# Optimization experiments

Hardware: AMD Instinct MI355X
Metric: run time of the kernel (lower is better)

## Reference

```python
import jax, jax.numpy as jnp
import numpy as np

# Tsit5 (Tsitouras 5(4)) Butcher tableau. 5th-order solution weights b == a7 row (FSAL).
A21 = 0.161
A31, A32 = -0.008480655492356989, 0.335480655492357
A41, A42, A43 = 2.8971530571054935, -6.359448489975075, 4.3622954328695815
A51, A52, A53, A54 = 5.325864828439257, -11.748883564062828, 7.4955393428898365, -0.09249506636175525
A61, A62, A63, A64, A65 = 5.86145544294642, -12.92096931784711, 8.159367898576159, -0.071584973281401, -0.028269050394068383
B1, B2, B3, B4, B5, B6 = 0.09646076681806523, 0.01, 0.4798896504144996, 1.379008574103742, -3.290069515436081, 2.324710524099774

B_TRAJ, D_STATE, D_FORCE, WIDTH = 1024, 256, 256, 512
T0, T1 = 0.0, 1.0
N_STEPS = 60  # fixed step h = DT0*SECOND = 60/3600 = 1/60 hour
H = (T1 - T0) / N_STEPS


def setup_inputs() -> dict:
    key = jax.random.key(0)
    ks = jax.random.split(key, 8)
    din = D_STATE + D_FORCE
    x0 = jax.random.normal(ks[0], (B_TRAJ, D_STATE), jnp.float32)
    u_forced = jax.random.normal(ks[1], (B_TRAJ, D_FORCE), jnp.float32) * 0.1
    W1 = jax.random.normal(ks[2], (WIDTH, din), jnp.float32) / np.sqrt(din)
    b1 = jnp.zeros((WIDTH,), jnp.float32)
    W2 = jax.random.normal(ks[3], (WIDTH, WIDTH), jnp.float32) / np.sqrt(WIDTH)
    b2 = jnp.zeros((WIDTH,), jnp.float32)
    W3 = jax.random.normal(ks[4], (D_STATE, WIDTH), jnp.float32) / np.sqrt(WIDTH)
    b3 = jnp.zeros((D_STATE,), jnp.float32)
    return dict(x0=x0, u_forced=u_forced, W1=W1, b1=b1, W2=W2, b2=b2, W3=W3, b3=b3)


def reference(x0, u_forced, W1, b1, W2, b2, W3, b3):
    # Augmented system: branch 0 = forced trajectory, branch 1 = unforced (zero force).
    # y: (2, B, D_STATE); u: (2, B, D_FORCE)
    y0 = jnp.stack([x0, x0])
    u = jnp.stack([u_forced, jnp.zeros_like(u_forced)])

    def mlp(z):  # z: (2, B, din) -> (2, B, D_STATE); eqx.nn.MLP default relu
        h = jax.nn.relu(jnp.einsum('kbi,oi->kbo', z, W1) + b1)
        h = jax.nn.relu(jnp.einsum('kbi,oi->kbo', h, W2) + b2)
        return jnp.einsum('kbi,oi->kbo', h, W3) + b3

    def f(y):  # ForcedVectorField: mlp(hstack((x, u))) on both branches at once
        return mlp(jnp.concatenate([y, u], axis=-1))

    def tsit5_step(y, _):
        k1 = f(y)
        k2 = f(y + H * (A21 * k1))
        k3 = f(y + H * (A31 * k1 + A32 * k2))
        k4 = f(y + H * (A41 * k1 + A42 * k2 + A43 * k3))
        k5 = f(y + H * (A51 * k1 + A52 * k2 + A53 * k3 + A54 * k4))
        k6 = f(y + H * (A61 * k1 + A62 * k2 + A63 * k3 + A64 * k4 + A65 * k5))
        y_new = y + H * (B1 * k1 + B2 * k2 + B3 * k3 + B4 * k4 + B5 * k5 + B6 * k6)
        return y_new, None

    y_final, _ = jax.lax.scan(jax.checkpoint(tsit5_step), y0, None, length=N_STEPS)
    # (forced_state, unforced_state) at t1, stacked: (2, B, D_STATE)
    return y_final
```

## Files before the change

kernel.cpp:

```cpp
#include <hip/hip_runtime.h>
#include <hip/hip_bf16.h>

typedef short  short8  __attribute__((ext_vector_type(8)));
typedef float  float4v __attribute__((ext_vector_type(4)));

#define NSTEPS 60
#define ROWS   16
#define GRID   128
#define C1S    518

constexpr double Hd = 1.0 / 60.0;
constexpr float HA1[1] = { (float)(Hd * 0.161) };
constexpr float HA2[2] = { (float)(Hd * -0.008480655492356989), (float)(Hd * 0.335480655492357) };
constexpr float HA3[3] = { (float)(Hd * 2.8971530571054935), (float)(Hd * -6.359448489975075),
                           (float)(Hd * 4.3622954328695815) };
constexpr float HA4[4] = { (float)(Hd * 5.325864828439257), (float)(Hd * -11.748883564062828),
                           (float)(Hd * 7.4955393428898365), (float)(Hd * -0.09249506636175525) };
constexpr float HA5[5] = { (float)(Hd * 5.86145544294642), (float)(Hd * -12.92096931784711),
                           (float)(Hd * 8.159367898576159), (float)(Hd * -0.071584973281401),
                           (float)(Hd * -0.028269050394068383) };
constexpr float HB6[6] = { (float)(Hd * 0.09646076681806523), (float)(Hd * 0.01),
                           (float)(Hd * 0.4798896504144996), (float)(Hd * 1.379008574103742),
                           (float)(Hd * -3.290069515436081), (float)(Hd * 2.324710524099774) };

__device__ __forceinline__ unsigned short f2bf(float f) {
    union { float f; unsigned u; } v; v.f = f;
    unsigned r = v.u + 0x7fffu + ((v.u >> 16) & 1u);
    return (unsigned short)(r >> 16);
}

__global__ void wconv(const float* __restrict__ W1, const float* __restrict__ W2,
                      const float* __restrict__ W3, unsigned short* __restrict__ ws) {
    int g = blockIdx.x * blockDim.x + threadIdx.x;
    int blk = g >> 6, l = g & 63;
    const float* src;
    if (blk < 256) {
        int b = blk; int nt = b >> 3, ks = b & 7;
        int n = nt * 16 + (l & 15), k = ks * 32 + (l >> 4) * 8;
        src = W1 + n * 512 + k;
    } else if (blk < 768) {
        int b = blk - 256; int nt = b >> 4, ks = b & 15;
        int n = nt * 16 + (l & 15), k = ks * 32 + (l >> 4) * 8;
        src = W2 + n * 512 + k;
    } else {
        int b = blk - 768; int nt = b >> 4, ks = b & 15;
        int n = nt * 16 + (l & 15), k = ks * 32 + (l >> 4) * 8;
        src = W3 + n * 512 + k;
    }
    short8 v;
#pragma unroll
    for (int j = 0; j < 8; ++j) v[j] = (short)f2bf(src[j]);
    *(((short8*)ws) + g) = v;
}

template<int KDIM, int NT>
__device__ __forceinline__ void mfma_block(const unsigned short* __restrict__ lds, int stride,
                                           const short8* __restrict__ wb, int ntg0, int lane,
                                           float4v* acc) {
    constexpr int KS = KDIM / 32;
    const int row  = lane & 15;
    const int koff = (lane >> 4) * 8;
    const int rm   = (row & 7) << 3;
    const short8* wp = wb + (size_t)ntg0 * KS * 64 + lane;
    short8 a_cur = *(const short8*)(lds + row * stride + (koff ^ rm));
    short8 b_cur[NT];
#pragma unroll
    for (int nt = 0; nt < NT; ++nt) b_cur[nt] = wp[(size_t)nt * KS * 64];
#pragma unroll
    for (int ks = 0; ks < KS; ++ks) {
        short8 a_nxt;
        short8 b_nxt[NT];
        if (ks + 1 < KS) {
            a_nxt = *(const short8*)(lds + row * stride + (((ks + 1) * 32 + koff) ^ rm));
#pragma unroll
            for (int nt = 0; nt < NT; ++nt) b_nxt[nt] = wp[((size_t)nt * KS + ks + 1) * 64];
        }
#pragma unroll
        for (int nt = 0; nt < NT; ++nt)
            acc[nt] = __builtin_amdgcn_mfma_f32_16x16x32_bf16(a_cur, b_cur[nt], acc[nt], 0, 0, 0);
        a_cur = a_nxt;
#pragma unroll
        for (int nt = 0; nt < NT; ++nt) b_cur[nt] = b_nxt[nt];
    }
}

__global__ void __launch_bounds__(512, 1) odeint(
        const float* __restrict__ x0, const float* __restrict__ uf,
        const float* __restrict__ W1, const float* __restrict__ b1,
        const float* __restrict__ b2, const float* __restrict__ b3,
        const unsigned short* __restrict__ ws, float* __restrict__ out) {
    __shared__ unsigned short xb[16 * 256];
    __shared__ unsigned short h1[16 * 512];
    __shared__ unsigned short h2[16 * 512];
    __shared__ float c1s[16 * C1S];
    __shared__ float bias2[512];
    __shared__ float bias3[256];

    const int tid  = threadIdx.x;
    const int wave = tid >> 6, lane = tid & 63;
    const int r0   = blockIdx.x * ROWS;

    float* utmp = (float*)h1;
    {
        const bool forced = (r0 < 1024);
        float4v* ud = (float4v*)utmp;
        for (int i = tid; i < ROWS * 64; i += 512) {
            int row = i >> 6, c4 = i & 63;
            float4v v = {0.f, 0.f, 0.f, 0.f};
            if (forced) v = *(const float4v*)(uf + (size_t)(r0 + row) * 256 + c4 * 4);
            ud[i] = v;
        }
    }
    bias2[tid] = b2[tid];
    if (tid < 256) bias3[tid] = b3[tid];
    __syncthreads();

    {
        int n = tid;
        float acc16[ROWS];
        float bb = b1[n];
#pragma unroll
        for (int r = 0; r < ROWS; ++r) acc16[r] = bb;
        const float* wrow = W1 + n * 512 + 256;
        for (int k = 0; k < 256; ++k) {
            float w = wrow[k];
#pragma unroll
            for (int r = 0; r < ROWS; ++r) acc16[r] += w * utmp[r * 256 + k];
        }
#pragma unroll
        for (int r = 0; r < ROWS; ++r) c1s[r * C1S + n] = acc16[r];
    }
    __syncthreads();

    float ybr[8];
    float kreg[6][8];
#pragma unroll
    for (int e = 0; e < 8; ++e) {
        int nt = e >> 2, r = e & 3;
        int row = (lane >> 4) * 4 + r;
        int n   = (wave * 2 + nt) * 16 + (lane & 15);
        ybr[e] = x0[(size_t)((r0 + row) & 1023) * 256 + n];
    }

    const short8* wy1 = (const short8*)ws;
    const short8* w2  = (const short8*)(ws + 131072);
    const short8* w3  = (const short8*)(ws + 393216);

#define DO_STAGE(S, COEF) do {                                                          \
    {                \
        _Pragma("unroll")                                                               \
        for (int e = 0; e < 8; ++e) {                                                   \
            int nt_ = e >> 2, r_ = e & 3;                                               \
            int row_ = (lane >> 4) * 4 + r_;                                            \
            int n_   = (wave * 2 + nt_) * 16 + (lane & 15);                             \
            float v_ = ybr[e];                                                          \
            _Pragma("unroll")                                                           \
            for (int j = 0; j < S; ++j) v_ += COEF[j] * kreg[j][e];                     \
            xb[row_ * 256 + (n_ ^ ((row_ & 7) << 3))] = f2bf(v_);                       \
        }                                                                               \
    }                                                                                   \
    __syncthreads();                                                   \
    {                                      \
        float4v a1[4];                                                                  \
        _Pragma("unroll") for (int q = 0; q < 4; ++q) a1[q] = (float4v){0.f,0.f,0.f,0.f}; \
        mfma_block<256, 4>(xb, 256, wy1, wave * 4, lane, a1);                           \
        _Pragma("unroll")                                                               \
        for (int nt = 0; nt < 4; ++nt) {                                                \
            int n_g = (wave * 4 + nt) * 16 + (lane & 15);                               \
            _Pragma("unroll")                                                           \
            for (int r = 0; r < 4; ++r) {                                               \
                int row = (lane >> 4) * 4 + r;                                          \
                float v = a1[nt][r] + c1s[row * C1S + n_g];                             \
                v = fmaxf(v, 0.f);                                                      \
                h1[row * 512 + (n_g ^ ((row & 7) << 3))] = f2bf(v);                     \
            }                                                                           \
        }                                                                               \
    }                                                                                   \
    __syncthreads();                                                   \
    {    \
        float4v a2[4];                                                                  \
        _Pragma("unroll") for (int q = 0; q < 4; ++q) a2[q] = (float4v){0.f,0.f,0.f,0.f}; \
        mfma_block<512, 4>(h1, 512, w2, wave * 4, lane, a2);                            \
        _Pragma("unroll")                                                               \
        for (int nt = 0; nt < 4; ++nt) {                                                \
            int n_g = (wave * 4 + nt) * 16 + (lane & 15);                               \
            _Pragma("unroll")                                                           \
            for (int r = 0; r < 4; ++r) {                                               \
                int row = (lane >> 4) * 4 + r;                                          \
                float v = a2[nt][r] + bias2[n_g];                                       \
                v = fmaxf(v, 0.f);                                                      \
                h2[row * 512 + (n_g ^ ((row & 7) << 3))] = f2bf(v);                     \
            }                                                                           \
        }                                                                               \
    }                                                                                   \
    __syncthreads();   \
    {        \
        float4v a3[2];                                                                  \
        _Pragma("unroll") for (int q = 0; q < 2; ++q) a3[q] = (float4v){0.f,0.f,0.f,0.f}; \
        mfma_block<512, 2>(h2, 512, w3, wave * 2, lane, a3);                            \
        _Pragma("unroll")                                                               \
        for (int nt = 0; nt < 2; ++nt) {                                                \
            int n_g = (wave * 2 + nt) * 16 + (lane & 15);                               \
            _Pragma("unroll")                                                           \
            for (int r = 0; r < 4; ++r) {                                               \
                kreg[S][nt * 4 + r] = a3[nt][r] + bias3[n_g];                           \
            }                                                                           \
        }                                                                               \
    }                                                                                   \
} while (0)

    for (int step = 0; step < NSTEPS; ++step) {
        DO_STAGE(0, HA1);
        DO_STAGE(1, HA1);
        DO_STAGE(2, HA2);
        DO_STAGE(3, HA3);
        DO_STAGE(4, HA4);
        DO_STAGE(5, HA5);
        {
#pragma unroll
            for (int e = 0; e < 8; ++e) {
                float v = ybr[e];
#pragma unroll
                for (int j = 0; j < 6; ++j) v += HB6[j] * kreg[j][e];
                ybr[e] = v;
            }
        }
    }
#undef DO_STAGE

#pragma unroll
    for (int e = 0; e < 8; ++e) {
        int nt = e >> 2, r = e & 3;
        int row = (lane >> 4) * 4 + r;
        int n   = (wave * 2 + nt) * 16 + (lane & 15);
        out[(size_t)(r0 + row) * 256 + n] = ybr[e];
    }
}

extern "C" void kernel_launch(void* const* d_in, const int* in_sizes, int n_in,
                              void* d_out, int out_size, void* d_ws, size_t ws_size,
                              hipStream_t stream) {
    const float* x0 = (const float*)d_in[0];
    const float* uf = (const float*)d_in[1];
    const float* W1 = (const float*)d_in[2];
    const float* b1 = (const float*)d_in[3];
    const float* W2 = (const float*)d_in[4];
    const float* b2 = (const float*)d_in[5];
    const float* W3 = (const float*)d_in[6];
    const float* b3 = (const float*)d_in[7];
    unsigned short* ws = (unsigned short*)d_ws;

    wconv<<<128, 512, 0, stream>>>(W1, W2, W3, ws);
    odeint<<<GRID, 512, 0, stream>>>(x0, uf, W1, b1, b2, b3, ws, (float*)d_out);
}
```

Before: 12.02 ms.

## Halve rows per block to double grid and raise occupancy bound

Each block now handles 8 trajectory rows instead of 16, so the grid doubles to 256 blocks and more CUs are covered. The 16-row MFMA tile is kept, with the upper 8 rows duplicated and their results discarded, which wastes half the matrix throughput and doubles weight traffic per row. Biases are moved from LDS into registers, LDS footprint shrinks, launch bounds allow several blocks per CU, and the MFMA loop drops its manual software prefetch.

```diff
diff --git a/kernel.cpp b/kernel.cpp
--- a/kernel.cpp
+++ b/kernel.cpp
@@ -5,8 +5,8 @@
 typedef float  float4v __attribute__((ext_vector_type(4)));
 
 #define NSTEPS 60
-#define ROWS   16
-#define GRID   128
+#define ROWS   8
+#define GRID   256
 #define C1S    518
 
 constexpr double Hd = 1.0 / 60.0;
@@ -53,93 +53,82 @@
     *(((short8*)ws) + g) = v;
 }
 
-template<int KDIM, int NT>
-__device__ __forceinline__ void mfma_block(const unsigned short* __restrict__ lds, int stride,
-                                           const short8* __restrict__ wb, int ntg0, int lane,
-                                           float4v* acc) {
+template<int KDIM>
+__device__ __forceinline__ void mfma2(const unsigned short* __restrict__ lds, int stride,
+                                      const short8* __restrict__ wb, int ntg0, int lane,
+                                      float4v* acc) {
     constexpr int KS = KDIM / 32;
-    const int row  = lane & 15;
+    const int vrow = lane & 7;
     const int koff = (lane >> 4) * 8;
-    const int rm   = (row & 7) << 3;
+    const int rm   = vrow << 3;
     const short8* wp = wb + (size_t)ntg0 * KS * 64 + lane;
-    short8 a_cur = *(const short8*)(lds + row * stride + (koff ^ rm));
-    short8 b_cur[NT];
-#pragma unroll
-    for (int nt = 0; nt < NT; ++nt) b_cur[nt] = wp[(size_t)nt * KS * 64];
 #pragma unroll
     for (int ks = 0; ks < KS; ++ks) {
-        short8 a_nxt;
-        short8 b_nxt[NT];
-        if (ks + 1 < KS) {
-            a_nxt = *(const short8*)(lds + row * stride + (((ks + 1) * 32 + koff) ^ rm));
-#pragma unroll
-            for (int nt = 0; nt < NT; ++nt) b_nxt[nt] = wp[((size_t)nt * KS + ks + 1) * 64];
-        }
-#pragma unroll
-        for (int nt = 0; nt < NT; ++nt)
-            acc[nt] = __builtin_amdgcn_mfma_f32_16x16x32_bf16(a_cur, b_cur[nt], acc[nt], 0, 0, 0);
-        a_cur = a_nxt;
-#pragma unroll
-        for (int nt = 0; nt < NT; ++nt) b_cur[nt] = b_nxt[nt];
-    }
-}
-
-__global__ void __launch_bounds__(512, 1) odeint(
+        short8 a  = *(const short8*)(lds + vrow * stride + (((ks * 32) + koff) ^ rm));
+        short8 b0 = wp[(size_t)ks * 64];
+        short8 b1 = wp[(size_t)(KS + ks) * 64];
+        acc[0] = __builtin_amdgcn_mfma_f32_16x16x32_bf16(a, b0, acc[0], 0, 0, 0);
+        acc[1] = __builtin_amdgcn_mfma_f32_16x16x32_bf16(a, b1, acc[1], 0, 0, 0);
+    }
+}
+
+__global__ void __launch_bounds__(512, 4) odeint(
         const float* __restrict__ x0, const float* __restrict__ uf,
         const float* __restrict__ W1, const float* __restrict__ b1,
         const float* __restrict__ b2, const float* __restrict__ b3,
         const unsigned short* __restrict__ ws, float* __restrict__ out) {
-    __shared__ unsigned short xb[16 * 256];
-    __shared__ unsigned short h1[16 * 512];
-    __shared__ unsigned short h2[16 * 512];
-    __shared__ float c1s[16 * C1S];
-    __shared__ float bias2[512];
-    __shared__ float bias3[256];
+    __shared__ unsigned short xb[8 * 256];
+    __shared__ unsigned short h1[8 * 512];
+    __shared__ unsigned short h2[8 * 512];
+    __shared__ float c1s[8 * C1S];
 
     const int tid  = threadIdx.x;
     const int wave = tid >> 6, lane = tid & 63;
     const int r0   = blockIdx.x * ROWS;
+    const bool forced = (r0 < 1024);
 
     float* utmp = (float*)h1;
     {
-        const bool forced = (r0 < 1024);
         float4v* ud = (float4v*)utmp;
         for (int i = tid; i < ROWS * 64; i += 512) {
-            int row = i >> 6, c4 = i & 63;
             float4v v = {0.f, 0.f, 0.f, 0.f};
-            if (forced) v = *(const float4v*)(uf + (size_t)(r0 + row) * 256 + c4 * 4);
+            if (forced) v = *(const float4v*)(uf + (size_t)(r0 + (i >> 6)) * 256 + (i & 63) * 4);
             ud[i] = v;
         }
     }
-    bias2[tid] = b2[tid];
-    if (tid < 256) bias3[tid] = b3[tid];
     __syncthreads();
 
     {
         int n = tid;
-        float acc16[ROWS];
+        float acc8[ROWS];
         float bb = b1[n];
 #pragma unroll
-        for (int r = 0; r < ROWS; ++r) acc16[r] = bb;
+        for (int r = 0; r < ROWS; ++r) acc8[r] = bb;
         const float* wrow = W1 + n * 512 + 256;
         for (int k = 0; k < 256; ++k) {
             float w = wrow[k];
 #pragma unroll
-            for (int r = 0; r < ROWS; ++r) acc16[r] += w * utmp[r * 256 + k];
+            for (int r = 0; r < ROWS; ++r) acc8[r] += w * utmp[r * 256 + k];
         }
 #pragma unroll
-        for (int r = 0; r < ROWS; ++r) c1s[r * C1S + n] = acc16[r];
+        for (int r = 0; r < ROWS; ++r) c1s[r * C1S + n] = acc8[r];
     }
     __syncthreads();
+
+    float breg2[4], breg3[2];
+#pragma unroll
+    for (int j = 0; j < 4; ++j) breg2[j] = b2[(wave * 4 + j) * 16 + (lane & 15)];
+#pragma unroll
+    for (int nt = 0; nt < 2; ++nt) breg3[nt] = b3[(wave * 2 + nt) * 16 + (lane & 15)];
 
     float ybr[8];
     float kreg[6][8];
 #pragma unroll
     for (int e = 0; e < 8; ++e) {
         int nt = e >> 2, r = e & 3;
-        int row = (lane >> 4) * 4 + r;
-        int n   = (wave * 2 + nt) * 16 + (lane & 15);
-        ybr[e] = x0[(size_t)((r0 + row) & 1023) * 256 + n];
+        int vrow = ((lane >> 4) * 4 + r) & 7;
+        int n    = (wave * 2 + nt) * 16 + (lane & 15);
+        ybr[e] = x0[(size_t)((r0 + vrow) & 1023) * 256 + n];
     }
 
     const short8* wy1 = (const short8*)ws;
@@ -147,7 +136,7 @@
     const short8* w3  = (const short8*)(ws + 393216);
 
 #define DO_STAGE(S, COEF) do {                                                          \
-    {                \
+    {                   \
         _Pragma("unroll")                                                               \
         for (int e = 0; e < 8; ++e) {                                                   \
             int nt_ = e >> 2, r_ = e & 3;                                               \
@@ -156,54 +145,58 @@
             float v_ = ybr[e];                                                          \
             _Pragma("unroll")                                                           \
             for (int j = 0; j < S; ++j) v_ += COEF[j] * kreg[j][e];                     \
-            xb[row_ * 256 + (n_ ^ ((row_ & 7) << 3))] = f2bf(v_);                       \
+            if (row_ < 8) xb[row_ * 256 + (n_ ^ (row_ << 3))] = f2bf(v_);               \
         }                                                                               \
     }                                                                                   \
     __syncthreads();                                                   \
-    {                                      \
-        float4v a1[4];                                                                  \
-        _Pragma("unroll") for (int q = 0; q < 4; ++q) a1[q] = (float4v){0.f,0.f,0.f,0.f}; \
-        mfma_block<256, 4>(xb, 256, wy1, wave * 4, lane, a1);                           \
-        _Pragma("unroll")                                                               \
-        for (int nt = 0; nt < 4; ++nt) {                                                \
-            int n_g = (wave * 4 + nt) * 16 + (lane & 15);                               \
+    {                     \
+        _Pragma("unroll")                                                               \
+        for (int p = 0; p < 2; ++p) {                                                   \
+            float4v a1[2] = {{0.f,0.f,0.f,0.f},{0.f,0.f,0.f,0.f}};                      \
+            mfma2<256>(xb, 256, wy1, wave * 4 + p * 2, lane, a1);                       \
+            _Pragma("unroll")                                                           \
+            for (int nt = 0; nt < 2; ++nt) {                                            \
+                int n_g = (wave * 4 + p * 2 + nt) * 16 + (lane & 15);                   \
+                _Pragma("unroll")                                                       \
+                for (int r = 0; r < 4; ++r) {                                           \
+                    int row = (lane >> 4) * 4 + r;                                      \
+                    if (row < 8) {                                                      \
+                        float v = a1[nt][r] + c1s[row * C1S + n_g];                     \
+                        h1[row * 512 + (n_g ^ (row << 3))] = f2bf(fmaxf(v, 0.f));       \
+                    }                                                                   \
+                }                                                                       \
+            }                                                                           \
+        }                                                                               \
+    }                                                                                   \
+    __syncthreads();                                                   \
+    {                     \
+        _Pragma("unroll")                                                               \
+        for (int p = 0; p < 2; ++p) {                                                   \
+            float4v a2[2] = {{0.f,0.f,0.f,0.f},{0.f,0.f,0.f,0.f}};                      \
+            mfma2<512>(h1, 512, w2, wave * 4 + p * 2, lane, a2);                        \
+            _Pragma("unroll")                                                           \
+            for (int nt = 0; nt < 2; ++nt) {                                            \
+                int n_g = (wave * 4 + p * 2 + nt) * 16 + (lane & 15);                   \
+                _Pragma("unroll")                                                       \
+                for (int r = 0; r < 4; ++r) {                                           \
+                    int row = (lane >> 4) * 4 + r;                                      \
+                    if (row < 8) {                                                      \
+                        float v = a2[nt][r] + breg2[p * 2 + nt];                        \
+                        h2[row * 512 + (n_g ^ (row << 3))] = f2bf(fmaxf(v, 0.f));       \
+                    }                                                                   \
+                }                                                                       \
+            }                                                                           \
+        }                                                                               \
+    }                                                                                   \
+    __syncthreads();                                                   \
+    {          \
+        float4v a3[2] = {{0.f,0.f,0.f,0.f},{0.f,0.f,0.f,0.f}};                          \
+        mfma2<512>(h2, 512, w3, wave * 2, lane, a3);                                    \
+        _Pragma("unroll")                                                               \
+        for (int nt = 0; nt < 2; ++nt) {                                                \
             _Pragma("unroll")                                                           \
             for (int r = 0; r < 4; ++r) {                                               \
-                int row = (lane >> 4) * 4 + r;                                          \
-                float v = a1[nt][r] + c1s[row * C1S + n_g];                             \
-                v = fmaxf(v, 0.f);                                                      \
-                h1[row * 512 + (n_g ^ ((row & 7) << 3))] = f2bf(v);                     \
-            }                                                                           \
-        }                                                                               \
-    }                                                                                   \
-    __syncthreads();                                                   \
-    {    \
-        float4v a2[4];                                                                  \
-        _Pragma("unroll") for (int q = 0; q < 4; ++q) a2[q] = (float4v){0.f,0.f,0.f,0.f}; \
-        mfma_block<512, 4>(h1, 512, w2, wave * 4, lane, a2);                            \
-        _Pragma("unroll")                                                               \
-        for (int nt = 0; nt < 4; ++nt) {                                                \
-            int n_g = (wave * 4 + nt) * 16 + (lane & 15);                               \
-            _Pragma("unroll")                                                           \
-            for (int r = 0; r < 4; ++r) {                                               \
-                int row = (lane >> 4) * 4 + r;                                          \
-                float v = a2[nt][r] + bias2[n_g];                                       \
-                v = fmaxf(v, 0.f);                                                      \
-                h2[row * 512 + (n_g ^ ((row & 7) << 3))] = f2bf(v);                     \
-            }                                                                           \
-        }                                                                               \
-    }                                                                                   \
-    __syncthreads();   \
-    {        \
-        float4v a3[2];                                                                  \
-        _Pragma("unroll") for (int q = 0; q < 2; ++q) a3[q] = (float4v){0.f,0.f,0.f,0.f}; \
-        mfma_block<512, 2>(h2, 512, w3, wave * 2, lane, a3);                            \
-        _Pragma("unroll")                                                               \
-        for (int nt = 0; nt < 2; ++nt) {                                                \
-            int n_g = (wave * 2 + nt) * 16 + (lane & 15);                               \
-            _Pragma("unroll")                                                           \
-            for (int r = 0; r < 4; ++r) {                                               \
-                kreg[S][nt * 4 + r] = a3[nt][r] + bias3[n_g];                           \
+                kreg[S][nt * 4 + r] = a3[nt][r] + breg3[nt];                            \
             }                                                                           \
         }                                                                               \
     }                                                                                   \
@@ -233,7 +226,7 @@
         int nt = e >> 2, r = e & 3;
         int row = (lane >> 4) * 4 + r;
         int n   = (wave * 2 + nt) * 16 + (lane & 15);
-        out[(size_t)(r0 + row) * 256 + n] = ybr[e];
+        if (row < 8) out[(size_t)(r0 + row) * 256 + n] = ybr[e];
     }
 }
 
```

Result: slower. 30.08 ms (+150.2%).
